# Kernel tuning notes

Measured on AMD Instinct MI355X. Metric: run time of the kernel, lower is better.

The kernel has to match this reference:

```python
import jax, jax.numpy as jnp
import numpy as np
import math

EPS = 1.0
N_IT = 10

def _sinkhorn_plan(C, eps, n_it):
    # C: [N, S, Sk] cost matrix; uniform marginals; log-domain Sinkhorn.
    n_rows, n_cols = C.shape[-2], C.shape[-1]
    log_mu = jnp.full(C.shape[:-1], -math.log(n_rows), C.dtype)
    log_nu = jnp.full(C.shape[:-2] + (n_cols,), -math.log(n_cols), C.dtype)

    def M(u, v):
        return (-C + u[..., :, None] + v[..., None, :]) / eps

    def body(carry, _):
        u, v = carry
        u = eps * (log_mu - jax.scipy.special.logsumexp(M(u, v), axis=-1)) + u
        v = eps * (log_nu - jax.scipy.special.logsumexp(M(u, v), axis=-2)) + v
        return (u, v), None

    u0 = jnp.zeros(C.shape[:-1], C.dtype)
    v0 = jnp.zeros(C.shape[:-2] + (C.shape[-1],), C.dtype)
    (u, v), _ = jax.lax.scan(body, (u0, v0), None, length=n_it)
    return jnp.exp(M(u, v))  # transport plan pi


def setup_inputs() -> dict:
    key = jax.random.key(0)
    kq, kk, kv = jax.random.split(key, 3)
    B, H, S, D = 2, 8, 1024, 64
    scale = 0.1  # keep exp(QK^T) numerically safe, as the model would via trained weights
    query = jax.random.normal(kq, (B, H, S, D), jnp.float32) * scale
    k_ = jax.random.normal(kk, (B, H, S, D), jnp.float32) * scale
    value = jax.random.normal(kv, (B, H, S, D), jnp.float32)
    return {"query": query, "key": k_, "value": value}


def reference(query, key, value):
    d = query.shape[-1]
    # exp-score attention (note: exp of raw QK^T, then divide by sqrt(d))
    scores = jnp.exp(jnp.einsum('bhqd,bhkd->bhqk', query, key)) / math.sqrt(d)
    B, H, S, Sk = scores.shape
    attn = scores.reshape(B * H, S, Sk)
    pi = _sinkhorn_plan(attn, EPS, N_IT)
    p_attn = (pi * Sk).reshape(B, H, S, Sk)  # row-stochastic doubly-normalized attention
    out = jnp.einsum('bhqk,bhkd->bhqd', p_attn, value)
    return out, p_attn
```

## Files before the change

kernel.cpp:

```cpp
#include <hip/hip_runtime.h>
#include <math.h>

#define NH   16
#define SEQ  1024
#define DIM  64
#define MUV  (1.0f/1024.0f)

typedef __attribute__((ext_vector_type(8))) short bf16x8;
typedef __attribute__((ext_vector_type(4))) float f32x4;

__device__ __forceinline__ float frcp(float x){ return __builtin_amdgcn_rcpf(x); }
__device__ __forceinline__ float bf2f(unsigned short u){
  union { unsigned int i; float f; } v; v.i = ((unsigned int)u) << 16; return v.f;
}
__device__ __forceinline__ unsigned short f2bf(float f){
  union { float f; unsigned int i; } v; v.f = f;
  return (unsigned short)((v.i + 0x7FFFu + ((v.i >> 16) & 1u)) >> 16);
}

__global__ __launch_bounds__(256) void prep_kernel(const float* __restrict__ Q,
                                                   const float* __restrict__ K,
                                                   const float* __restrict__ V,
                                                   unsigned short* __restrict__ Qbf,
                                                   unsigned short* __restrict__ Kbf,
                                                   unsigned short* __restrict__ Vt) {
  __shared__ float Vsh[64][68];
  const int h = blockIdx.y, ck = blockIdx.x, t = threadIdx.x;
  const int r = t >> 2, cp = (t & 3) * 16;
  const size_t gbase = ((size_t)h * SEQ + ck * 64 + r) * DIM + cp;
  {
    union { unsigned short u[16]; uint4 q[2]; } pk;
#pragma unroll
    for (int k = 0; k < 4; k++){
      const float4 v = *(const float4*)(Q + gbase + k * 4);
      pk.u[k*4+0]=f2bf(v.x); pk.u[k*4+1]=f2bf(v.y); pk.u[k*4+2]=f2bf(v.z); pk.u[k*4+3]=f2bf(v.w);
    }
    *(uint4*)(Qbf + gbase) = pk.q[0];
    *(uint4*)(Qbf + gbase + 8) = pk.q[1];
  }
  {
    union { unsigned short u[16]; uint4 q[2]; } pk;
#pragma unroll
    for (int k = 0; k < 4; k++){
      const float4 v = *(const float4*)(K + gbase + k * 4);
      pk.u[k*4+0]=f2bf(v.x); pk.u[k*4+1]=f2bf(v.y); pk.u[k*4+2]=f2bf(v.z); pk.u[k*4+3]=f2bf(v.w);
    }
    *(uint4*)(Kbf + gbase) = pk.q[0];
    *(uint4*)(Kbf + gbase + 8) = pk.q[1];
  }
  {
#pragma unroll
    for (int k = 0; k < 4; k++)
      *(float4*)&Vsh[r][cp + k * 4] = *(const float4*)(V + gbase + k * 4);
    __syncthreads();
    const int dd = t >> 2, jp = (t & 3) * 16;
    union { unsigned short u[16]; uint4 q[2]; } pk;
#pragma unroll
    for (int k = 0; k < 16; k++) pk.u[k] = f2bf(Vsh[jp + k][dd]);
    unsigned short* dst = Vt + ((size_t)h * DIM + dd) * SEQ + ck * 64 + jp;
    *(uint4*)dst       = pk.q[0];
    *(uint4*)(dst + 8) = pk.q[1];
  }
}

__global__ __launch_bounds__(256, 2)
void sink_rc(const unsigned short* __restrict__ Qbf,
             const unsigned short* __restrict__ Kbf,
             const float* __restrict__ cprev,
             float* __restrict__ cnext,
             float* __restrict__ avg,
             int first)
{
  __shared__ unsigned short Ksh[32 * 1024];
  __shared__ float bsh[1024];
  __shared__ float rsum[4][32];
  __shared__ float ash[32];
  const int h = blockIdx.y, ch = blockIdx.x, r0 = ch * 32, t = threadIdx.x;
  const int lane = t & 63, w = t >> 6, fr = lane & 15, fq = lane >> 4;

  if (first){
    *(float4*)&bsh[t * 4] = make_float4(1.f, 1.f, 1.f, 1.f);
  } else {
    float4 s = make_float4(0, 0, 0, 0);
    const float* cp = cprev + (size_t)h * 32 * 1024 + t * 4;
#pragma unroll 8
    for (int sl = 0; sl < 32; sl++){
      const float4 v = *(const float4*)(cp + (size_t)sl * 1024);
      s.x += v.x; s.y += v.y; s.z += v.z; s.w += v.w;
    }
    *(float4*)&bsh[t * 4] = make_float4(MUV * frcp(s.x), MUV * frcp(s.y),
                                        MUV * frcp(s.z), MUV * frcp(s.w));
  }
  __syncthreads();

  const unsigned short* qp = Qbf + ((size_t)h * SEQ + r0 + fr) * DIM + fq * 8;
  const bf16x8 qa00 = *(const bf16x8*)qp;
  const bf16x8 qa01 = *(const bf16x8*)(qp + 32);
  const bf16x8 qa10 = *(const bf16x8*)(qp + 16 * DIM);
  const bf16x8 qa11 = *(const bf16x8*)(qp + 16 * DIM + 32);

  float rp[8] = {0.f,0.f,0.f,0.f,0.f,0.f,0.f,0.f};

#pragma unroll 2
  for (int cc = 0; cc < 16; cc++){
    const int c0 = cc * 64 + w * 16;
    const unsigned short* kp = Kbf + ((size_t)h * SEQ + c0 + fr) * DIM + fq * 8;
    const bf16x8 kb0 = *(const bf16x8*)kp;
    const bf16x8 kb1 = *(const bf16x8*)(kp + 32);
    f32x4 a0 = {0.f,0.f,0.f,0.f}, a1 = {0.f,0.f,0.f,0.f};
    a0 = __builtin_amdgcn_mfma_f32_16x16x32_bf16(qa00, kb0, a0, 0, 0, 0);
    a0 = __builtin_amdgcn_mfma_f32_16x16x32_bf16(qa01, kb1, a0, 0, 0, 0);
    a1 = __builtin_amdgcn_mfma_f32_16x16x32_bf16(qa10, kb0, a1, 0, 0, 0);
    a1 = __builtin_amdgcn_mfma_f32_16x16x32_bf16(qa11, kb1, a1, 0, 0, 0);
    const float bcol = bsh[c0 + fr];
    const int col2 = (c0 + fr) * 2;
#pragma unroll
    for (int r = 0; r < 4; r++){
      const int row0 = fq * 4 + r;
      const float kv0 = __expf(-0.125f * __expf(a0[r]));
      const unsigned short ku0 = f2bf(kv0);
      *(unsigned short*)((char*)Ksh + row0 * 2048 + (col2 ^ ((row0 & 7) << 4))) = ku0;
      rp[r] += bf2f(ku0) * bcol;
      const int row1 = 16 + fq * 4 + r;
      const float kv1 = __expf(-0.125f * __expf(a1[r]));
      const unsigned short ku1 = f2bf(kv1);
      *(unsigned short*)((char*)Ksh + row1 * 2048 + (col2 ^ ((row1 & 7) << 4))) = ku1;
      rp[4 + r] += bf2f(ku1) * bcol;
    }
  }

#pragma unroll
  for (int m = 1; m <= 8; m <<= 1){
#pragma unroll
    for (int i = 0; i < 8; i++) rp[i] += __shfl_xor(rp[i], m);
  }
  if (fr == 0){
#pragma unroll
    for (int r = 0; r < 4; r++){
      rsum[w][fq * 4 + r]      = rp[r];
      rsum[w][16 + fq * 4 + r] = rp[4 + r];
    }
  }
  __syncthreads();
  if (t < 32){
    const float rs = rsum[0][t] + rsum[1][t] + rsum[2][t] + rsum[3][t];
    const float a = MUV * frcp(rs);
    ash[t] = a;
    avg[h * SEQ + r0 + t] = a;
  }
  __syncthreads();

  float4 ca = make_float4(0, 0, 0, 0);
  const int bo = t * 8;
#pragma unroll 8
  for (int i = 0; i < 32; i++){
    const ushort4 k4 = *(const ushort4*)((char*)Ksh + i * 2048 + (bo ^ ((i & 7) << 4)));
    const float a = ash[i];
    ca.x += bf2f(k4.x) * a; ca.y += bf2f(k4.y) * a;
    ca.z += bf2f(k4.z) * a; ca.w += bf2f(k4.w) * a;
  }
  *(float4*)(cnext + ((size_t)h * 32 + ch) * 1024 + t * 4) = ca;
}

__global__ __launch_bounds__(256, 2)
void final_rc(const unsigned short* __restrict__ Qbf,
              const unsigned short* __restrict__ Kbf,
              const unsigned short* __restrict__ Vt,
              const float* __restrict__ cpart,
              const float* __restrict__ avg,
              float* __restrict__ Pmat,
              float* __restrict__ out)
{
  __shared__ unsigned short Ksh[32 * 1024];
  __shared__ float bsh[1024];
  __shared__ float ash[32];
  const int h = blockIdx.y, ch = blockIdx.x, r0 = ch * 32, t = threadIdx.x;
  const int lane = t & 63, w = t >> 6, fr = lane & 15, fq = lane >> 4;

  {
    float4 s = make_float4(0, 0, 0, 0);
    const float* cp = cpart + (size_t)h * 32 * 1024 + t * 4;
#pragma unroll 8
    for (int sl = 0; sl < 32; sl++){
      const float4 v = *(const float4*)(cp + (size_t)sl * 1024);
      s.x += v.x; s.y += v.y; s.z += v.z; s.w += v.w;
    }
    *(float4*)&bsh[t * 4] = make_float4(MUV * frcp(s.x), MUV * frcp(s.y),
                                        MUV * frcp(s.z), MUV * frcp(s.w));
  }
  if (t < 32) ash[t] = 1024.f * avg[h * SEQ + r0 + t];

  const unsigned short* qp = Qbf + ((size_t)h * SEQ + r0 + fr) * DIM + fq * 8;
  const bf16x8 qa00 = *(const bf16x8*)qp;
  const bf16x8 qa01 = *(const bf16x8*)(qp + 32);
  const bf16x8 qa10 = *(const bf16x8*)(qp + 16 * DIM);
  const bf16x8 qa11 = *(const bf16x8*)(qp + 16 * DIM + 32);

#pragma unroll 2
  for (int cc = 0; cc < 16; cc++){
    const int c0 = cc * 64 + w * 16;
    const unsigned short* kp = Kbf + ((size_t)h * SEQ + c0 + fr) * DIM + fq * 8;
    const bf16x8 kb0 = *(const bf16x8*)kp;
    const bf16x8 kb1 = *(const bf16x8*)(kp + 32);
    f32x4 a0 = {0.f,0.f,0.f,0.f}, a1 = {0.f,0.f,0.f,0.f};
    a0 = __builtin_amdgcn_mfma_f32_16x16x32_bf16(qa00, kb0, a0, 0, 0, 0);
    a0 = __builtin_amdgcn_mfma_f32_16x16x32_bf16(qa01, kb1, a0, 0, 0, 0);
    a1 = __builtin_amdgcn_mfma_f32_16x16x32_bf16(qa10, kb0, a1, 0, 0, 0);
    a1 = __builtin_amdgcn_mfma_f32_16x16x32_bf16(qa11, kb1, a1, 0, 0, 0);
    const int col2 = (c0 + fr) * 2;
#pragma unroll
    for (int r = 0; r < 4; r++){
      const int row0 = fq * 4 + r;
      *(unsigned short*)((char*)Ksh + row0 * 2048 + (col2 ^ ((row0 & 7) << 4))) =
          f2bf(__expf(-0.125f * __expf(a0[r])));
      const int row1 = 16 + fq * 4 + r;
      *(unsigned short*)((char*)Ksh + row1 * 2048 + (col2 ^ ((row1 & 7) << 4))) =
          f2bf(__expf(-0.125f * __expf(a1[r])));
    }
  }
  __syncthreads();

  {
    const int prow = t >> 3, pc = t & 7;
    const float ar = ash[prow];
    const int swp = (prow & 7) << 4;
    float* pg = Pmat + ((size_t)h * SEQ + r0 + prow) * SEQ;
#pragma unroll
    for (int p16 = 0; p16 < 16; p16++){
      const int colb = (p16 * 8 + pc) * 8;
      const uint4 kq = *(const uint4*)((char*)Ksh + prow * 2048 + ((colb * 2) ^ swp));
      const float4 b0 = *(const float4*)&bsh[colb];
      const float4 b1 = *(const float4*)&bsh[colb + 4];
      float4 o0, o1;
      o0.x = ar * b0.x * bf2f((unsigned short)(kq.x));
      o0.y = ar * b0.y * bf2f((unsigned short)(kq.x >> 16));
      o0.z = ar * b0.z * bf2f((unsigned short)(kq.y));
      o0.w = ar * b0.w * bf2f((unsigned short)(kq.y >> 16));
      o1.x = ar * b1.x * bf2f((unsigned short)(kq.z));
      o1.y = ar * b1.y * bf2f((unsigned short)(kq.z >> 16));
      o1.z = ar * b1.z * bf2f((unsigned short)(kq.w));
      o1.w = ar * b1.w * bf2f((unsigned short)(kq.w >> 16));
      *(float4*)(pg + colb)     = o0;
      *(float4*)(pg + colb + 4) = o1;
    }
  }

  f32x4 o0 = {0.f,0.f,0.f,0.f}, o1 = {0.f,0.f,0.f,0.f};
  const float ar0 = ash[fr];
  const float ar1 = ash[16 + fr];
  const int sw0 = (fr & 7) << 4;
  const char* kr0 = (const char*)Ksh + fr * 2048;
  const char* kr1 = (const char*)Ksh + (16 + fr) * 2048;
  const unsigned short* vp = Vt + ((size_t)h * DIM + w * 16 + fr) * SEQ;
#pragma unroll 2
  for (int jc = 0; jc < 32; jc++){
    const int jb = jc * 32 + fq * 8;
    const bf16x8 vb = *(const bf16x8*)(vp + jb);
    const float4 b0 = *(const float4*)&bsh[jb];
    const float4 b1 = *(const float4*)&bsh[jb + 4];
    const float bv[8] = {b0.x, b0.y, b0.z, b0.w, b1.x, b1.y, b1.z, b1.w};
    const bf16x8 k0 = *(const bf16x8*)(kr0 + ((jb * 2) ^ sw0));
    const bf16x8 k1 = *(const bf16x8*)(kr1 + ((jb * 2) ^ sw0));
    union { unsigned short u[8]; bf16x8 v; } pa0, pa1;
#pragma unroll
    for (int e = 0; e < 8; e++){
      pa0.u[e] = f2bf(ar0 * bv[e] * bf2f((unsigned short)k0[e]));
      pa1.u[e] = f2bf(ar1 * bv[e] * bf2f((unsigned short)k1[e]));
    }
    o0 = __builtin_amdgcn_mfma_f32_16x16x32_bf16(pa0.v, vb, o0, 0, 0, 0);
    o1 = __builtin_amdgcn_mfma_f32_16x16x32_bf16(pa1.v, vb, o1, 0, 0, 0);
  }

  float* og = out + ((size_t)h * SEQ + r0) * DIM + w * 16 + fr;
#pragma unroll
  for (int r = 0; r < 4; r++)
    og[(size_t)(fq * 4 + r) * DIM] = o0[r];
  float* og1 = og + (size_t)16 * DIM;
#pragma unroll
  for (int r = 0; r < 4; r++)
    og1[(size_t)(fq * 4 + r) * DIM] = o1[r];
}

extern "C" void kernel_launch(void* const* d_in, const int* in_sizes, int n_in,
                              void* d_out, int out_size, void* d_ws, size_t ws_size,
                              hipStream_t stream) {
  (void)in_sizes; (void)n_in; (void)out_size; (void)ws_size;
  const float* Q = (const float*)d_in[0];
  const float* K = (const float*)d_in[1];
  const float* V = (const float*)d_in[2];
  float* out  = (float*)d_out;
  float* Pmat = out + (size_t)NH * SEQ * DIM;

  unsigned short* Qbf = (unsigned short*)d_ws;
  unsigned short* Kbf = Qbf + (size_t)NH * SEQ * DIM;
  unsigned short* Vt  = Kbf + (size_t)NH * SEQ * DIM;
  float* cp0 = (float*)(Vt + (size_t)NH * SEQ * DIM);
  float* cp1 = cp0 + (size_t)NH * 32 * SEQ;
  float* avg = cp1 + (size_t)NH * 32 * SEQ;

  prep_kernel<<<dim3(16, 16), 256, 0, stream>>>(Q, K, V, Qbf, Kbf, Vt);
  for (int it = 0; it < 10; it++){
    const float* cprev = (it & 1) ? cp0 : cp1;
    float*       cnext = (it & 1) ? cp1 : cp0;
    sink_rc<<<dim3(32, 16), 256, 0, stream>>>(Qbf, Kbf, cprev, cnext, avg, it == 0 ? 1 : 0);
  }
  final_rc<<<dim3(32, 16), 256, 0, stream>>>(Qbf, Kbf, Vt, cp1, avg, Pmat, out);
}
```

Measured before the change: 271.5 us.

## Halve row tile, accumulate column sums atomically with rotating triple buffer

The Sinkhorn row-block per workgroup shrinks from 32 to 16 rows, doubling the grid and raising the occupancy hint. The Gibbs kernel values are now kept in registers instead of LDS. Column partial sums are reduced through shuffles and atomically added into a single per-head vector, and a rotating three-buffer scheme zeroes the next accumulator. This removes the 32-slice partial-sum reread at the start of each iteration. The final kernel computes P directly from the MFMA output, writes it, and stages bf16 P in LDS for the PV product, at the cost of atomic contention and less coalesced Pmat stores.

```diff
diff --git a/kernel.cpp b/kernel.cpp
--- a/kernel.cpp
+++ b/kernel.cpp
@@ -63,222 +63,165 @@
   }
 }
 
-__global__ __launch_bounds__(256, 2)
+__global__ __launch_bounds__(256, 4)
 void sink_rc(const unsigned short* __restrict__ Qbf,
              const unsigned short* __restrict__ Kbf,
              const float* __restrict__ cprev,
              float* __restrict__ cnext,
+             float* __restrict__ zer,
              float* __restrict__ avg,
              int first)
 {
-  __shared__ unsigned short Ksh[32 * 1024];
   __shared__ float bsh[1024];
-  __shared__ float rsum[4][32];
-  __shared__ float ash[32];
-  const int h = blockIdx.y, ch = blockIdx.x, r0 = ch * 32, t = threadIdx.x;
+  __shared__ float csh[1024];
+  __shared__ float rsum[4][16];
+  __shared__ float ash[16];
+  const int h = blockIdx.y, ch = blockIdx.x, r0 = ch * 16, t = threadIdx.x;
   const int lane = t & 63, w = t >> 6, fr = lane & 15, fq = lane >> 4;
+
+  if (t < 16) zer[h * SEQ + ch * 16 + t] = 0.f;
 
   if (first){
     *(float4*)&bsh[t * 4] = make_float4(1.f, 1.f, 1.f, 1.f);
   } else {
-    float4 s = make_float4(0, 0, 0, 0);
-    const float* cp = cprev + (size_t)h * 32 * 1024 + t * 4;
-#pragma unroll 8
-    for (int sl = 0; sl < 32; sl++){
-      const float4 v = *(const float4*)(cp + (size_t)sl * 1024);
-      s.x += v.x; s.y += v.y; s.z += v.z; s.w += v.w;
-    }
-    *(float4*)&bsh[t * 4] = make_float4(MUV * frcp(s.x), MUV * frcp(s.y),
-                                        MUV * frcp(s.z), MUV * frcp(s.w));
-  }
-  __syncthreads();
-
-  const unsigned short* qp = Qbf + ((size_t)h * SEQ + r0 + fr) * DIM + fq * 8;
-  const bf16x8 qa00 = *(const bf16x8*)qp;
-  const bf16x8 qa01 = *(const bf16x8*)(qp + 32);
-  const bf16x8 qa10 = *(const bf16x8*)(qp + 16 * DIM);
-  const bf16x8 qa11 = *(const bf16x8*)(qp + 16 * DIM + 32);
-
-  float rp[8] = {0.f,0.f,0.f,0.f,0.f,0.f,0.f,0.f};
-
-#pragma unroll 2
+    const float4 c4 = *(const float4*)(cprev + h * SEQ + t * 4);
+    *(float4*)&bsh[t * 4] = make_float4(MUV * frcp(c4.x), MUV * frcp(c4.y),
+                                        MUV * frcp(c4.z), MUV * frcp(c4.w));
+  }
+  __syncthreads();
+
+  const unsigned short* qp = Qbf + ((size_t)(h * SEQ) + r0 + fr) * DIM + fq * 8;
+  const bf16x8 qa0 = *(const bf16x8*)qp;
+  const bf16x8 qa1 = *(const bf16x8*)(qp + 32);
+
+  unsigned int kx0[16], kx1[16];
+  float rp0 = 0.f, rp1 = 0.f, rp2 = 0.f, rp3 = 0.f;
+
+#pragma unroll
   for (int cc = 0; cc < 16; cc++){
     const int c0 = cc * 64 + w * 16;
-    const unsigned short* kp = Kbf + ((size_t)h * SEQ + c0 + fr) * DIM + fq * 8;
+    const unsigned short* kp = Kbf + ((size_t)(h * SEQ) + c0 + fr) * DIM + fq * 8;
     const bf16x8 kb0 = *(const bf16x8*)kp;
     const bf16x8 kb1 = *(const bf16x8*)(kp + 32);
-    f32x4 a0 = {0.f,0.f,0.f,0.f}, a1 = {0.f,0.f,0.f,0.f};
-    a0 = __builtin_amdgcn_mfma_f32_16x16x32_bf16(qa00, kb0, a0, 0, 0, 0);
-    a0 = __builtin_amdgcn_mfma_f32_16x16x32_bf16(qa01, kb1, a0, 0, 0, 0);
-    a1 = __builtin_amdgcn_mfma_f32_16x16x32_bf16(qa10, kb0, a1, 0, 0, 0);
-    a1 = __builtin_amdgcn_mfma_f32_16x16x32_bf16(qa11, kb1, a1, 0, 0, 0);
-    const float bcol = bsh[c0 + fr];
-    const int col2 = (c0 + fr) * 2;
-#pragma unroll
-    for (int r = 0; r < 4; r++){
-      const int row0 = fq * 4 + r;
-      const float kv0 = __expf(-0.125f * __expf(a0[r]));
-      const unsigned short ku0 = f2bf(kv0);
-      *(unsigned short*)((char*)Ksh + row0 * 2048 + (col2 ^ ((row0 & 7) << 4))) = ku0;
-      rp[r] += bf2f(ku0) * bcol;
-      const int row1 = 16 + fq * 4 + r;
-      const float kv1 = __expf(-0.125f * __expf(a1[r]));
-      const unsigned short ku1 = f2bf(kv1);
-      *(unsigned short*)((char*)Ksh + row1 * 2048 + (col2 ^ ((row1 & 7) << 4))) = ku1;
-      rp[4 + r] += bf2f(ku1) * bcol;
-    }
+    f32x4 a = {0.f, 0.f, 0.f, 0.f};
+    a = __builtin_amdgcn_mfma_f32_16x16x32_bf16(qa0, kb0, a, 0, 0, 0);
+    a = __builtin_amdgcn_mfma_f32_16x16x32_bf16(qa1, kb1, a, 0, 0, 0);
+    const float bc = bsh[c0 + fr];
+    const float k0 = __expf(-0.125f * __expf(a[0]));
+    const float k1 = __expf(-0.125f * __expf(a[1]));
+    const float k2 = __expf(-0.125f * __expf(a[2]));
+    const float k3 = __expf(-0.125f * __expf(a[3]));
+    rp0 += k0 * bc; rp1 += k1 * bc; rp2 += k2 * bc; rp3 += k3 * bc;
+    kx0[cc] = (unsigned int)f2bf(k0) | ((unsigned int)f2bf(k1) << 16);
+    kx1[cc] = (unsigned int)f2bf(k2) | ((unsigned int)f2bf(k3) << 16);
   }
 
 #pragma unroll
   for (int m = 1; m <= 8; m <<= 1){
-#pragma unroll
-    for (int i = 0; i < 8; i++) rp[i] += __shfl_xor(rp[i], m);
+    rp0 += __shfl_xor(rp0, m); rp1 += __shfl_xor(rp1, m);
+    rp2 += __shfl_xor(rp2, m); rp3 += __shfl_xor(rp3, m);
   }
   if (fr == 0){
-#pragma unroll
-    for (int r = 0; r < 4; r++){
-      rsum[w][fq * 4 + r]      = rp[r];
-      rsum[w][16 + fq * 4 + r] = rp[4 + r];
-    }
-  }
-  __syncthreads();
-  if (t < 32){
+    rsum[w][fq * 4 + 0] = rp0; rsum[w][fq * 4 + 1] = rp1;
+    rsum[w][fq * 4 + 2] = rp2; rsum[w][fq * 4 + 3] = rp3;
+  }
+  __syncthreads();
+  if (t < 16){
     const float rs = rsum[0][t] + rsum[1][t] + rsum[2][t] + rsum[3][t];
-    const float a = MUV * frcp(rs);
-    ash[t] = a;
-    avg[h * SEQ + r0 + t] = a;
-  }
-  __syncthreads();
-
-  float4 ca = make_float4(0, 0, 0, 0);
-  const int bo = t * 8;
-#pragma unroll 8
-  for (int i = 0; i < 32; i++){
-    const ushort4 k4 = *(const ushort4*)((char*)Ksh + i * 2048 + (bo ^ ((i & 7) << 4)));
-    const float a = ash[i];
-    ca.x += bf2f(k4.x) * a; ca.y += bf2f(k4.y) * a;
-    ca.z += bf2f(k4.z) * a; ca.w += bf2f(k4.w) * a;
-  }
-  *(float4*)(cnext + ((size_t)h * 32 + ch) * 1024 + t * 4) = ca;
-}
-
-__global__ __launch_bounds__(256, 2)
-void final_rc(const unsigned short* __restrict__ Qbf,
-              const unsigned short* __restrict__ Kbf,
-              const unsigned short* __restrict__ Vt,
-              const float* __restrict__ cpart,
-              const float* __restrict__ avg,
-              float* __restrict__ Pmat,
-              float* __restrict__ out)
+    const float a_ = MUV * frcp(rs);
+    ash[t] = a_;
+    avg[h * SEQ + r0 + t] = a_;
+  }
+  __syncthreads();
+
+  const float a0 = ash[fq * 4 + 0], a1 = ash[fq * 4 + 1];
+  const float a2 = ash[fq * 4 + 2], a3 = ash[fq * 4 + 3];
+#pragma unroll
+  for (int cc = 0; cc < 16; cc++){
+    float cp = a0 * bf2f((unsigned short)kx0[cc]) + a1 * bf2f((unsigned short)(kx0[cc] >> 16))
+             + a2 * bf2f((unsigned short)kx1[cc]) + a3 * bf2f((unsigned short)(kx1[cc] >> 16));
+    cp += __shfl_xor(cp, 16);
+    cp += __shfl_xor(cp, 32);
+    if (lane < 16) csh[cc * 64 + w * 16 + fr] = cp;
+  }
+  __syncthreads();
+  {
+    const float4 c4 = *(const float4*)&csh[t * 4];
+    float* dst = cnext + h * SEQ + t * 4;
+    atomicAdd(dst + 0, c4.x); atomicAdd(dst + 1, c4.y);
+    atomicAdd(dst + 2, c4.z); atomicAdd(dst + 3, c4.w);
+  }
+}
+
+__global__ __launch_bounds__(256, 4)
+void final_fused(const unsigned short* __restrict__ Qbf,
+                 const unsigned short* __restrict__ Kbf,
+                 const unsigned short* __restrict__ Vt,
+                 const float* __restrict__ cfin,
+                 const float* __restrict__ avg,
+                 float* __restrict__ Pmat,
+                 float* __restrict__ out)
 {
-  __shared__ unsigned short Ksh[32 * 1024];
+  __shared__ unsigned short Psh[16 * 1024];
   __shared__ float bsh[1024];
-  __shared__ float ash[32];
-  const int h = blockIdx.y, ch = blockIdx.x, r0 = ch * 32, t = threadIdx.x;
+  __shared__ float ash[16];
+  const int h = blockIdx.y, ch = blockIdx.x, r0 = ch * 16, t = threadIdx.x;
   const int lane = t & 63, w = t >> 6, fr = lane & 15, fq = lane >> 4;
 
   {
-    float4 s = make_float4(0, 0, 0, 0);
-    const float* cp = cpart + (size_t)h * 32 * 1024 + t * 4;
-#pragma unroll 8
-    for (int sl = 0; sl < 32; sl++){
-      const float4 v = *(const float4*)(cp + (size_t)sl * 1024);
-      s.x += v.x; s.y += v.y; s.z += v.z; s.w += v.w;
-    }
-    *(float4*)&bsh[t * 4] = make_float4(MUV * frcp(s.x), MUV * frcp(s.y),
-                                        MUV * frcp(s.z), MUV * frcp(s.w));
-  }
-  if (t < 32) ash[t] = 1024.f * avg[h * SEQ + r0 + t];
-
-  const unsigned short* qp = Qbf + ((size_t)h * SEQ + r0 + fr) * DIM + fq * 8;
-  const bf16x8 qa00 = *(const bf16x8*)qp;
-  const bf16x8 qa01 = *(const bf16x8*)(qp + 32);
-  const bf16x8 qa10 = *(const bf16x8*)(qp + 16 * DIM);
-  const bf16x8 qa11 = *(const bf16x8*)(qp + 16 * DIM + 32);
-
-#pragma unroll 2
+    const float4 c4 = *(const float4*)(cfin + h * SEQ + t * 4);
+    *(float4*)&bsh[t * 4] = make_float4(MUV * frcp(c4.x), MUV * frcp(c4.y),
+                                        MUV * frcp(c4.z), MUV * frcp(c4.w));
+  }
+  if (t < 16) ash[t] = 1024.f * avg[h * SEQ + r0 + t];
+  __syncthreads();
+
+  const float ar0 = ash[fq * 4 + 0], ar1 = ash[fq * 4 + 1];
+  const float ar2 = ash[fq * 4 + 2], ar3 = ash[fq * 4 + 3];
+
+  const unsigned short* qp = Qbf + ((size_t)(h * SEQ) + r0 + fr) * DIM + fq * 8;
+  const bf16x8 qa0 = *(const bf16x8*)qp;
+  const bf16x8 qa1 = *(const bf16x8*)(qp + 32);
+
+#pragma unroll
   for (int cc = 0; cc < 16; cc++){
     const int c0 = cc * 64 + w * 16;
-    const unsigned short* kp = Kbf + ((size_t)h * SEQ + c0 + fr) * DIM + fq * 8;
+    const unsigned short* kp = Kbf + ((size_t)(h * SEQ) + c0 + fr) * DIM + fq * 8;
     const bf16x8 kb0 = *(const bf16x8*)kp;
     const bf16x8 kb1 = *(const bf16x8*)(kp + 32);
-    f32x4 a0 = {0.f,0.f,0.f,0.f}, a1 = {0.f,0.f,0.f,0.f};
-    a0 = __builtin_amdgcn_mfma_f32_16x16x32_bf16(qa00, kb0, a0, 0, 0, 0);
-    a0 = __builtin_amdgcn_mfma_f32_16x16x32_bf16(qa01, kb1, a0, 0, 0, 0);
-    a1 = __builtin_amdgcn_mfma_f32_16x16x32_bf16(qa10, kb0, a1, 0, 0, 0);
-    a1 = __builtin_amdgcn_mfma_f32_16x16x32_bf16(qa11, kb1, a1, 0, 0, 0);
+    f32x4 a = {0.f, 0.f, 0.f, 0.f};
+    a = __builtin_amdgcn_mfma_f32_16x16x32_bf16(qa0, kb0, a, 0, 0, 0);
+    a = __builtin_amdgcn_mfma_f32_16x16x32_bf16(qa1, kb1, a, 0, 0, 0);
+    const float bc = bsh[c0 + fr];
+    const float p0 = ar0 * bc * __expf(-0.125f * __expf(a[0]));
+    const float p1 = ar1 * bc * __expf(-0.125f * __expf(a[1]));
+    const float p2 = ar2 * bc * __expf(-0.125f * __expf(a[2]));
+    const float p3 = ar3 * bc * __expf(-0.125f * __expf(a[3]));
+    float* pg = Pmat + ((size_t)(h * SEQ) + r0 + fq * 4) * SEQ + c0 + fr;
+    pg[0 * SEQ] = p0; pg[1 * SEQ] = p1; pg[2 * SEQ] = p2; pg[3 * SEQ] = p3;
     const int col2 = (c0 + fr) * 2;
-#pragma unroll
-    for (int r = 0; r < 4; r++){
-      const int row0 = fq * 4 + r;
-      *(unsigned short*)((char*)Ksh + row0 * 2048 + (col2 ^ ((row0 & 7) << 4))) =
-          f2bf(__expf(-0.125f * __expf(a0[r])));
-      const int row1 = 16 + fq * 4 + r;
-      *(unsigned short*)((char*)Ksh + row1 * 2048 + (col2 ^ ((row1 & 7) << 4))) =
-          f2bf(__expf(-0.125f * __expf(a1[r])));
-    }
-  }
-  __syncthreads();
-
-  {
-    const int prow = t >> 3, pc = t & 7;
-    const float ar = ash[prow];
-    const int swp = (prow & 7) << 4;
-    float* pg = Pmat + ((size_t)h * SEQ + r0 + prow) * SEQ;
-#pragma unroll
-    for (int p16 = 0; p16 < 16; p16++){
-      const int colb = (p16 * 8 + pc) * 8;
-      const uint4 kq = *(const uint4*)((char*)Ksh + prow * 2048 + ((colb * 2) ^ swp));
-      const float4 b0 = *(const float4*)&bsh[colb];
-      const float4 b1 = *(const float4*)&bsh[colb + 4];
-      float4 o0, o1;
-      o0.x = ar * b0.x * bf2f((unsigned short)(kq.x));
-      o0.y = ar * b0.y * bf2f((unsigned short)(kq.x >> 16));
-      o0.z = ar * b0.z * bf2f((unsigned short)(kq.y));
-      o0.w = ar * b0.w * bf2f((unsigned short)(kq.y >> 16));
-      o1.x = ar * b1.x * bf2f((unsigned short)(kq.z));
-      o1.y = ar * b1.y * bf2f((unsigned short)(kq.z >> 16));
-      o1.z = ar * b1.z * bf2f((unsigned short)(kq.w));
-      o1.w = ar * b1.w * bf2f((unsigned short)(kq.w >> 16));
-      *(float4*)(pg + colb)     = o0;
-      *(float4*)(pg + colb + 4) = o1;
-    }
-  }
-
-  f32x4 o0 = {0.f,0.f,0.f,0.f}, o1 = {0.f,0.f,0.f,0.f};
-  const float ar0 = ash[fr];
-  const float ar1 = ash[16 + fr];
-  const int sw0 = (fr & 7) << 4;
-  const char* kr0 = (const char*)Ksh + fr * 2048;
-  const char* kr1 = (const char*)Ksh + (16 + fr) * 2048;
+    const int row0 = fq * 4;
+    *(unsigned short*)((char*)Psh + (row0    ) * 2048 + (col2 ^ (((row0    ) & 7) << 4))) = f2bf(p0);
+    *(unsigned short*)((char*)Psh + (row0 + 1) * 2048 + (col2 ^ (((row0 + 1) & 7) << 4))) = f2bf(p1);
+    *(unsigned short*)((char*)Psh + (row0 + 2) * 2048 + (col2 ^ (((row0 + 2) & 7) << 4))) = f2bf(p2);
+    *(unsigned short*)((char*)Psh + (row0 + 3) * 2048 + (col2 ^ (((row0 + 3) & 7) << 4))) = f2bf(p3);
+  }
+  __syncthreads();
+
+  f32x4 o = {0.f, 0.f, 0.f, 0.f};
   const unsigned short* vp = Vt + ((size_t)h * DIM + w * 16 + fr) * SEQ;
-#pragma unroll 2
+  const char* pr = (const char*)Psh + fr * 2048;
+  const int sw = (fr & 7) << 4;
+#pragma unroll 8
   for (int jc = 0; jc < 32; jc++){
     const int jb = jc * 32 + fq * 8;
+    const bf16x8 pa = *(const bf16x8*)(pr + ((jb * 2) ^ sw));
     const bf16x8 vb = *(const bf16x8*)(vp + jb);
-    const float4 b0 = *(const float4*)&bsh[jb];
-    const float4 b1 = *(const float4*)&bsh[jb + 4];
-    const float bv[8] = {b0.x, b0.y, b0.z, b0.w, b1.x, b1.y, b1.z, b1.w};
-    const bf16x8 k0 = *(const bf16x8*)(kr0 + ((jb * 2) ^ sw0));
-    const bf16x8 k1 = *(const bf16x8*)(kr1 + ((jb * 2) ^ sw0));
-    union { unsigned short u[8]; bf16x8 v; } pa0, pa1;
-#pragma unroll
-    for (int e = 0; e < 8; e++){
-      pa0.u[e] = f2bf(ar0 * bv[e] * bf2f((unsigned short)k0[e]));
-      pa1.u[e] = f2bf(ar1 * bv[e] * bf2f((unsigned short)k1[e]));
-    }
-    o0 = __builtin_amdgcn_mfma_f32_16x16x32_bf16(pa0.v, vb, o0, 0, 0, 0);
-    o1 = __builtin_amdgcn_mfma_f32_16x16x32_bf16(pa1.v, vb, o1, 0, 0, 0);
-  }
-
-  float* og = out + ((size_t)h * SEQ + r0) * DIM + w * 16 + fr;
-#pragma unroll
-  for (int r = 0; r < 4; r++)
-    og[(size_t)(fq * 4 + r) * DIM] = o0[r];
-  float* og1 = og + (size_t)16 * DIM;
-#pragma unroll
-  for (int r = 0; r < 4; r++)
-    og1[(size_t)(fq * 4 + r) * DIM] = o1[r];
+    o = __builtin_amdgcn_mfma_f32_16x16x32_bf16(pa, vb, o, 0, 0, 0);
+  }
+
+  float* og = out + ((size_t)(h * SEQ) + r0 + fq * 4) * DIM + w * 16 + fr;
+  og[0 * DIM] = o[0]; og[1 * DIM] = o[1]; og[2 * DIM] = o[2]; og[3 * DIM] = o[3];
 }
 
 extern "C" void kernel_launch(void* const* d_in, const int* in_sizes, int n_in,
@@ -294,15 +237,17 @@
   unsigned short* Qbf = (unsigned short*)d_ws;
   unsigned short* Kbf = Qbf + (size_t)NH * SEQ * DIM;
   unsigned short* Vt  = Kbf + (size_t)NH * SEQ * DIM;
-  float* cp0 = (float*)(Vt + (size_t)NH * SEQ * DIM);
-  float* cp1 = cp0 + (size_t)NH * 32 * SEQ;
-  float* avg = cp1 + (size_t)NH * 32 * SEQ;
+  float* cbuf = (float*)(Vt + (size_t)NH * SEQ * DIM);
+  float* avg  = cbuf + (size_t)3 * NH * SEQ;
 
   prep_kernel<<<dim3(16, 16), 256, 0, stream>>>(Q, K, V, Qbf, Kbf, Vt);
+  hipMemsetAsync(cbuf + (size_t)NH * SEQ, 0, (size_t)NH * SEQ * sizeof(float), stream);
   for (int it = 0; it < 10; it++){
-    const float* cprev = (it & 1) ? cp0 : cp1;
-    float*       cnext = (it & 1) ? cp1 : cp0;
-    sink_rc<<<dim3(32, 16), 256, 0, stream>>>(Qbf, Kbf, cprev, cnext, avg, it == 0 ? 1 : 0);
-  }
-  final_rc<<<dim3(32, 16), 256, 0, stream>>>(Qbf, Kbf, Vt, cp1, avg, Pmat, out);
-}
+    float* crd = cbuf + (size_t)(it % 3) * NH * SEQ;
+    float* cac = cbuf + (size_t)((it + 1) % 3) * NH * SEQ;
+    float* czr = cbuf + (size_t)((it + 2) % 3) * NH * SEQ;
+    sink_rc<<<dim3(64, 16), 256, 0, stream>>>(Qbf, Kbf, crd, cac, czr, avg, it == 0 ? 1 : 0);
+  }
+  float* cfin = cbuf + (size_t)((10) % 3) * NH * SEQ;
+  final_fused<<<dim3(64, 16), 256, 0, stream>>>(Qbf, Kbf, Vt, cfin, avg, Pmat, out);
+}
```

New measurement: 439.1 us. 61.7% more time.
